# Performance work log

Hardware: AMD Instinct MI355X
Metric: run time of the kernel (lower is better)

## Reference

```python
import jax, jax.numpy as jnp
import numpy as np

GRID_SIZE = 5
SPLINE_ORDER = 3
GRID_RANGE = (-1.0, 1.0)
IN_FEATURES = 1024
OUT_FEATURES = 1024
N_TOKENS = 8192
N_BASIS = GRID_SIZE + SPLINE_ORDER  # number of B-spline basis functions per input feature


def make_grid(dtype=jnp.float32):
    # Extended knot vector: grid_size+1 interior knots over grid_range, padded by
    # spline_order knots on each side (efficient-KAN convention; the intended
    # semantics of the TF port's b_splines recursion).
    h = (GRID_RANGE[1] - GRID_RANGE[0]) / GRID_SIZE
    idx = jnp.arange(-SPLINE_ORDER, GRID_SIZE + SPLINE_ORDER + 1, dtype=dtype)
    return idx * h + GRID_RANGE[0]  # [grid_size + 2*spline_order + 1]


def b_splines(x, grid):
    # x: [N, in] -> bases: [N, in, N_BASIS] via de Boor / Cox recursion.
    x3 = x[..., None]  # [N, in, 1]
    g = grid  # [K], broadcasts against last axis
    bases = ((x3 >= g[:-1]) & (x3 < g[1:])).astype(x.dtype)  # order-0: [N, in, K-1]
    for k in range(1, SPLINE_ORDER + 1):
        left = (x3 - g[: -(k + 1)]) / (g[k:-1] - g[: -(k + 1)])
        right = (g[k + 1:] - x3) / (g[k + 1:] - g[1:-k])
        bases = left * bases[..., :-1] + right * bases[..., 1:]
    return bases  # [N, in, N_BASIS]


def setup_inputs() -> dict:
    key = jax.random.key(0)
    k1, k2, k3, k4 = jax.random.split(key, 4)
    x = jax.random.uniform(k1, (N_TOKENS, IN_FEATURES), dtype=jnp.float32)
    base_weight = jax.random.normal(k2, (IN_FEATURES, OUT_FEATURES), dtype=jnp.float32) * 0.02
    spline_weight = jax.random.normal(k3, (OUT_FEATURES, IN_FEATURES, N_BASIS), dtype=jnp.float32) * 0.02
    spline_scaler = jax.random.normal(k4, (OUT_FEATURES, IN_FEATURES), dtype=jnp.float32) * 0.1
    return {"x": x, "base_weight": base_weight, "spline_weight": spline_weight,
            "spline_scaler": spline_scaler}


def reference(x, base_weight, spline_weight, spline_scaler):
    grid = make_grid(x.dtype)
    # base path: silu(x) @ W_base
    base_out = jnp.matmul(jax.nn.silu(x), base_weight)  # [N, out]
    # spline path: grouped contraction over (in_feature, basis)
    bases = b_splines(x, grid)  # [N, in, nb]
    sw = spline_weight * spline_scaler[..., None]  # standalone scale: [out, in, nb]
    spline_out = jnp.einsum('nib,oib->no', bases, sw)
    return base_out + spline_out  # [N, out]
```

## Files before the change

### kernel.cpp

```cpp
#include <hip/hip_runtime.h>
#include <hip/hip_bf16.h>
#include <stdint.h>

typedef unsigned short u16;
typedef __attribute__((ext_vector_type(8))) __bf16 bf16x8;
typedef __attribute__((ext_vector_type(4))) float f32x4;

#define NTOK 8192
#define NIN  1024
#define NOUT 1024
#define KTOT 9216

__device__ __forceinline__ u16 f2bf(float f) {
  union { float f; unsigned u; } v; v.f = f;
  unsigned r = v.u + 0x7FFFu + ((v.u >> 16) & 1u);
  return (u16)(r >> 16);
}

__device__ __forceinline__ void gload_lds16(const void* g, void* l) {
  __builtin_amdgcn_global_load_lds(
      (__attribute__((address_space(1))) void*)(uintptr_t)g,
      (__attribute__((address_space(3))) void*)(uintptr_t)l, 16, 0, 0);
}

__global__ void prep_base(const float* __restrict__ W, u16* __restrict__ Bt) {
  __shared__ float tile[32][33];
  int i0 = blockIdx.x * 32, o0 = blockIdx.y * 32;
  int tx = threadIdx.x, ty = threadIdx.y;
#pragma unroll
  for (int r = 0; r < 4; ++r)
    tile[ty + 8 * r][tx] = W[(size_t)(i0 + ty + 8 * r) * NOUT + o0 + tx];
  __syncthreads();
#pragma unroll
  for (int r = 0; r < 4; ++r)
    Bt[(size_t)(o0 + ty + 8 * r) * KTOT + i0 + tx] = f2bf(tile[tx][ty + 8 * r]);
}

__global__ void prep_spline(const float* __restrict__ SW, const float* __restrict__ SS,
                            u16* __restrict__ Bt) {
  int idx = blockIdx.x * 256 + threadIdx.x;
  int o = idx >> 10, i = idx & 1023;
  float s = SS[idx];
  const float4* p = (const float4*)(SW + (size_t)idx * 8);
  float4 a = p[0], b = p[1];
  union { u16 us[8]; uint4 v; } pk;
  pk.us[0] = f2bf(a.x * s); pk.us[1] = f2bf(a.y * s);
  pk.us[2] = f2bf(a.z * s); pk.us[3] = f2bf(a.w * s);
  pk.us[4] = f2bf(b.x * s); pk.us[5] = f2bf(b.y * s);
  pk.us[6] = f2bf(b.z * s); pk.us[7] = f2bf(b.w * s);
  *(uint4*)(Bt + (size_t)o * KTOT + NIN + (size_t)i * 8) = pk.v;
}

__global__ void build_a(const float* __restrict__ X, u16* __restrict__ A) {
  int idx = blockIdx.x * 256 + threadIdx.x;
  int n = idx >> 10, i = idx & 1023;
  float x = X[idx];
  float sx = x / (1.f + expf(-x));
  A[(size_t)n * KTOT + i] = f2bf(sx);
  float bb[11];
#pragma unroll
  for (int j = 0; j < 11; ++j) {
    float gj  = 0.4f * j - 2.2f;
    float gj1 = 0.4f * (j + 1) - 2.2f;
    bb[j] = (x >= gj && x < gj1) ? 1.f : 0.f;
  }
#pragma unroll
  for (int k = 1; k <= 3; ++k) {
    float inv = 1.f / (0.4f * k);
#pragma unroll
    for (int j = 0; j + k < 11; ++j) {
      float gj = 0.4f * j - 2.2f;
      float left  = (x - gj) * inv;
      float right = (0.4f * (j + k + 1) - 2.2f - x) * inv;
      bb[j] = left * bb[j] + right * bb[j + 1];
    }
  }
  union { u16 us[8]; uint4 v; } pk;
#pragma unroll
  for (int j = 0; j < 8; ++j) pk.us[j] = f2bf(bb[j]);
  *(uint4*)(A + (size_t)n * KTOT + NIN + (size_t)i * 8) = pk.v;
}

__global__ __launch_bounds__(256, 2) void kan_gemm(const u16* __restrict__ A,
                                                   const u16* __restrict__ Bt,
                                                   float* __restrict__ C) {
  __shared__ u16 As[128 * 64];
  __shared__ u16 Bs[128 * 64];
  const int bid = blockIdx.x;
  const int logical = (bid & 7) * 64 + (bid >> 3);
  const int bn = logical >> 6;
  const int bm = logical & 63;
  const int tid = threadIdx.x;
  const int w = tid >> 6, l = tid & 63;
  const int wr = w >> 1, wc = w & 1;

  const u16* Ab = A  + (size_t)bm * 128 * KTOT;
  const u16* Bb = Bt + (size_t)bn * 128 * KTOT;

  f32x4 acc[4][4];
#pragma unroll
  for (int m = 0; m < 4; ++m)
#pragma unroll
    for (int n = 0; n < 4; ++n)
      acc[m][n] = f32x4{0.f, 0.f, 0.f, 0.f};

  int rr[4], gc8[4], lb[4];
#pragma unroll
  for (int it = 0; it < 4; ++it) {
    int c = it * 256 + tid;
    int r = c >> 3, s = c & 7;
    rr[it] = r;
    gc8[it] = (s ^ (r & 7)) * 8;
    lb[it] = (it * 256 + w * 64) * 8;
  }

  for (int k0 = 0; k0 < KTOT; k0 += 64) {
#pragma unroll
    for (int it = 0; it < 4; ++it)
      gload_lds16(Ab + (size_t)rr[it] * KTOT + k0 + gc8[it], &As[lb[it]]);
#pragma unroll
    for (int it = 0; it < 4; ++it)
      gload_lds16(Bb + (size_t)rr[it] * KTOT + k0 + gc8[it], &Bs[lb[it]]);
    __syncthreads();
#pragma unroll
    for (int kk = 0; kk < 2; ++kk) {
      bf16x8 af[4], bfr[4];
#pragma unroll
      for (int m = 0; m < 4; ++m) {
        int rA = wr * 64 + m * 16 + (l & 15);
        int ch = (kk * 4 + (l >> 4)) ^ (rA & 7);
        af[m] = *(const bf16x8*)&As[rA * 64 + ch * 8];
      }
#pragma unroll
      for (int n = 0; n < 4; ++n) {
        int rB = wc * 64 + n * 16 + (l & 15);
        int ch = (kk * 4 + (l >> 4)) ^ (rB & 7);
        bfr[n] = *(const bf16x8*)&Bs[rB * 64 + ch * 8];
      }
#pragma unroll
      for (int m = 0; m < 4; ++m)
#pragma unroll
        for (int n = 0; n < 4; ++n)
          acc[m][n] = __builtin_amdgcn_mfma_f32_16x16x32_bf16(af[m], bfr[n], acc[m][n], 0, 0, 0);
    }
    __syncthreads();
  }

  const int row0 = bm * 128 + wr * 64 + ((l >> 4) << 2);
  const int col0 = bn * 128 + wc * 64 + (l & 15);
#pragma unroll
  for (int m = 0; m < 4; ++m)
#pragma unroll
    for (int n = 0; n < 4; ++n) {
      float* cp = C + (size_t)(row0 + m * 16) * NOUT + col0 + n * 16;
#pragma unroll
      for (int r = 0; r < 4; ++r)
        cp[(size_t)r * NOUT] = acc[m][n][r];
    }
}

extern "C" void kernel_launch(void* const* d_in, const int* in_sizes, int n_in,
                              void* d_out, int out_size, void* d_ws, size_t ws_size,
                              hipStream_t stream) {
  const float* x  = (const float*)d_in[0];
  const float* bw = (const float*)d_in[1];
  const float* sw = (const float*)d_in[2];
  const float* ss = (const float*)d_in[3];
  float* out = (float*)d_out;

  u16* Bt = (u16*)d_ws;
  u16* A  = (u16*)((char*)d_ws + (size_t)NOUT * KTOT * 2);

  prep_base<<<dim3(32, 32), dim3(32, 8), 0, stream>>>(bw, Bt);
  prep_spline<<<(NOUT * NIN) / 256, 256, 0, stream>>>(sw, ss, Bt);
  build_a<<<(NTOK * NIN) / 256, 256, 0, stream>>>(x, A);
  kan_gemm<<<512, 256, 0, stream>>>(A, Bt, out);
}
```

Baseline: 324.1 us.

## Triple-buffer GEMM with 128x256 tiles, 8 waves, and split-phase prefetch

After: 289.0 us. 1.12x faster.

```diff
diff --git a/kernel.cpp b/kernel.cpp
--- a/kernel.cpp
+++ b/kernel.cpp
@@ -10,6 +10,13 @@
 #define NIN  1024
 #define NOUT 1024
 #define KTOT 9216
+#define BM 128
+#define BN 256
+#define BK 64
+#define NT (KTOT / BK)
+#define ABUF (BM * BK)
+#define BBUF (BN * BK)
+#define TBUF (ABUF + BBUF)
 
 __device__ __forceinline__ u16 f2bf(float f) {
   union { float f; unsigned u; } v; v.f = f;
@@ -22,6 +29,7 @@
       (__attribute__((address_space(1))) void*)(uintptr_t)g,
       (__attribute__((address_space(3))) void*)(uintptr_t)l, 16, 0, 0);
 }
+
 
 __global__ void prep_base(const float* __restrict__ W, u16* __restrict__ Bt) {
   __shared__ float tile[32][33];
@@ -55,7 +63,7 @@
   int idx = blockIdx.x * 256 + threadIdx.x;
   int n = idx >> 10, i = idx & 1023;
   float x = X[idx];
-  float sx = x / (1.f + expf(-x));
+  float sx = x / (1.f + __expf(-x));
   A[(size_t)n * KTOT + i] = f2bf(sx);
   float bb[11];
 #pragma unroll
@@ -81,21 +89,43 @@
   *(uint4*)(A + (size_t)n * KTOT + NIN + (size_t)i * 8) = pk.v;
 }
 
-__global__ __launch_bounds__(256, 2) void kan_gemm(const u16* __restrict__ A,
+
+__global__ __launch_bounds__(512, 2) void kan_gemm(const u16* __restrict__ A,
                                                    const u16* __restrict__ Bt,
                                                    float* __restrict__ C) {
-  __shared__ u16 As[128 * 64];
-  __shared__ u16 Bs[128 * 64];
-  const int bid = blockIdx.x;
-  const int logical = (bid & 7) * 64 + (bid >> 3);
-  const int bn = logical >> 6;
-  const int bm = logical & 63;
+  __shared__ u16 lds[3 * TBUF];
   const int tid = threadIdx.x;
   const int w = tid >> 6, l = tid & 63;
-  const int wr = w >> 1, wc = w & 1;
-
-  const u16* Ab = A  + (size_t)bm * 128 * KTOT;
-  const u16* Bb = Bt + (size_t)bn * 128 * KTOT;
+  const int wr = w >> 2, wc = w & 3;
+  const int l4 = l >> 4, lc = l & 15;
+
+  const int bid = blockIdx.x;
+  const int xcd = bid & 7, jj = bid >> 3;
+  const int bn = xcd >> 1;
+  const int bm = (xcd & 1) * 32 + jj;
+
+  const u16* Ab = A  + (size_t)bm * BM * KTOT;
+  const u16* Bb = Bt + (size_t)bn * BN * KTOT;
+
+  int srcA[2], dstA[2], srcB[4], dstB[4];
+#pragma unroll
+  for (int it = 0; it < 2; ++it) {
+    int c = it * 512 + tid, r = c >> 3, s = (c & 7) ^ (r & 7);
+    srcA[it] = r * KTOT + s * 8;
+    dstA[it] = (it * 512 + w * 64) * 8;
+  }
+#pragma unroll
+  for (int it = 0; it < 4; ++it) {
+    int c = it * 512 + tid, r = c >> 3, s = (c & 7) ^ (r & 7);
+    srcB[it] = r * KTOT + s * 8;
+    dstB[it] = ABUF + (it * 512 + w * 64) * 8;
+  }
+
+  int rA[4], rB[4];
+#pragma unroll
+  for (int m = 0; m < 4; ++m) rA[m] = wr * 64 + m * 16 + lc;
+#pragma unroll
+  for (int n = 0; n < 4; ++n) rB[n] = wc * 64 + n * 16 + lc;
 
   f32x4 acc[4][4];
 #pragma unroll
@@ -104,50 +134,85 @@
     for (int n = 0; n < 4; ++n)
       acc[m][n] = f32x4{0.f, 0.f, 0.f, 0.f};
 
-  int rr[4], gc8[4], lb[4];
-#pragma unroll
-  for (int it = 0; it < 4; ++it) {
-    int c = it * 256 + tid;
-    int r = c >> 3, s = c & 7;
-    rr[it] = r;
-    gc8[it] = (s ^ (r & 7)) * 8;
-    lb[it] = (it * 256 + w * 64) * 8;
-  }
-
-  for (int k0 = 0; k0 < KTOT; k0 += 64) {
-#pragma unroll
-    for (int it = 0; it < 4; ++it)
-      gload_lds16(Ab + (size_t)rr[it] * KTOT + k0 + gc8[it], &As[lb[it]]);
-#pragma unroll
-    for (int it = 0; it < 4; ++it)
-      gload_lds16(Bb + (size_t)rr[it] * KTOT + k0 + gc8[it], &Bs[lb[it]]);
-    __syncthreads();
-#pragma unroll
-    for (int kk = 0; kk < 2; ++kk) {
-      bf16x8 af[4], bfr[4];
-#pragma unroll
-      for (int m = 0; m < 4; ++m) {
-        int rA = wr * 64 + m * 16 + (l & 15);
-        int ch = (kk * 4 + (l >> 4)) ^ (rA & 7);
-        af[m] = *(const bf16x8*)&As[rA * 64 + ch * 8];
-      }
-#pragma unroll
-      for (int n = 0; n < 4; ++n) {
-        int rB = wc * 64 + n * 16 + (l & 15);
-        int ch = (kk * 4 + (l >> 4)) ^ (rB & 7);
-        bfr[n] = *(const bf16x8*)&Bs[rB * 64 + ch * 8];
-      }
-#pragma unroll
-      for (int m = 0; m < 4; ++m)
-#pragma unroll
-        for (int n = 0; n < 4; ++n)
-          acc[m][n] = __builtin_amdgcn_mfma_f32_16x16x32_bf16(af[m], bfr[n], acc[m][n], 0, 0, 0);
-    }
-    __syncthreads();
-  }
-
-  const int row0 = bm * 128 + wr * 64 + ((l >> 4) << 2);
-  const int col0 = bn * 128 + wc * 64 + (l & 15);
+#pragma unroll
+  for (int it = 0; it < 2; ++it) gload_lds16(Ab + srcA[it], &lds[dstA[it]]);
+#pragma unroll
+  for (int it = 0; it < 4; ++it) gload_lds16(Bb + srcB[it], &lds[dstB[it]]);
+#pragma unroll
+  for (int it = 0; it < 2; ++it) gload_lds16(Ab + srcA[it] + BK, &lds[TBUF + dstA[it]]);
+#pragma unroll
+  for (int it = 0; it < 4; ++it) gload_lds16(Bb + srcB[it] + BK, &lds[TBUF + dstB[it]]);
+  asm volatile("s_waitcnt vmcnt(6)" ::: "memory");
+  __builtin_amdgcn_s_barrier();
+
+  int cur = 0;
+  for (int t = 0; t < NT; ++t) {
+    const int curo = cur * TBUF;
+    const int nxto = ((cur == 0) ? 2 : cur - 1) * TBUF;
+    const bool pf = (t + 2) < NT;
+    const int k0n = (t + 2) * BK;
+
+    bf16x8 a_frag[4][2], b_frag[2][2];
+
+#pragma unroll
+    for (int m = 0; m < 4; ++m)
+#pragma unroll
+      for (int kk = 0; kk < 2; ++kk)
+        a_frag[m][kk] = *(const bf16x8*)&lds[curo + rA[m] * 64 + (((kk * 4 + l4) ^ (rA[m] & 7)) * 8)];
+#pragma unroll
+    for (int n = 0; n < 2; ++n)
+#pragma unroll
+      for (int kk = 0; kk < 2; ++kk)
+        b_frag[n][kk] = *(const bf16x8*)&lds[curo + ABUF + rB[n] * 64 + (((kk * 4 + l4) ^ (rB[n] & 7)) * 8)];
+    if (pf) {
+#pragma unroll
+      for (int it = 0; it < 2; ++it) gload_lds16(Ab + srcA[it] + k0n, &lds[nxto + dstA[it]]);
+      gload_lds16(Bb + srcB[0] + k0n, &lds[nxto + dstB[0]]);
+    }
+    __builtin_amdgcn_s_barrier();
+    asm volatile("s_waitcnt lgkmcnt(0)" ::: "memory");
+    __builtin_amdgcn_sched_barrier(0);
+    __builtin_amdgcn_s_setprio(1);
+#pragma unroll
+    for (int m = 0; m < 4; ++m)
+#pragma unroll
+      for (int n = 0; n < 2; ++n)
+#pragma unroll
+        for (int kk = 0; kk < 2; ++kk)
+          acc[m][n] = __builtin_amdgcn_mfma_f32_16x16x32_bf16(a_frag[m][kk], b_frag[n][kk], acc[m][n], 0, 0, 0);
+    __builtin_amdgcn_s_setprio(0);
+    __builtin_amdgcn_s_barrier();
+
+#pragma unroll
+    for (int n = 0; n < 2; ++n)
+#pragma unroll
+      for (int kk = 0; kk < 2; ++kk)
+        b_frag[n][kk] = *(const bf16x8*)&lds[curo + ABUF + rB[n + 2] * 64 + (((kk * 4 + l4) ^ (rB[n + 2] & 7)) * 8)];
+    if (pf) {
+#pragma unroll
+      for (int it = 1; it < 4; ++it) gload_lds16(Bb + srcB[it] + k0n, &lds[nxto + dstB[it]]);
+    }
+    __builtin_amdgcn_s_barrier();
+    asm volatile("s_waitcnt lgkmcnt(0)" ::: "memory");
+    __builtin_amdgcn_sched_barrier(0);
+    __builtin_amdgcn_s_setprio(1);
+#pragma unroll
+    for (int m = 0; m < 4; ++m)
+#pragma unroll
+      for (int n = 0; n < 2; ++n)
+#pragma unroll
+        for (int kk = 0; kk < 2; ++kk)
+          acc[m][n + 2] = __builtin_amdgcn_mfma_f32_16x16x32_bf16(a_frag[m][kk], b_frag[n][kk], acc[m][n + 2], 0, 0, 0);
+    __builtin_amdgcn_s_setprio(0);
+    if (t >= NT - 2) { asm volatile("s_waitcnt vmcnt(0)" ::: "memory"); }
+    else             { asm volatile("s_waitcnt vmcnt(6)" ::: "memory"); }
+    __builtin_amdgcn_s_barrier();
+
+    cur = (cur == 2) ? 0 : cur + 1;
+  }
+
+  const int row0 = bm * BM + wr * 64 + l4 * 4;
+  const int col0 = bn * BN + wc * 64 + lc;
 #pragma unroll
   for (int m = 0; m < 4; ++m)
 #pragma unroll
@@ -174,5 +239,5 @@
   prep_base<<<dim3(32, 32), dim3(32, 8), 0, stream>>>(bw, Bt);
   prep_spline<<<(NOUT * NIN) / 256, 256, 0, stream>>>(sw, ss, Bt);
   build_a<<<(NTOK * NIN) / 256, 256, 0, stream>>>(x, A);
-  kan_gemm<<<512, 256, 0, stream>>>(A, Bt, out);
-}
+  kan_gemm<<<256, 512, 0, stream>>>(A, Bt, out);
+}
```
